# Kernel tuning notes

Measured on AMD Instinct MI355X. Metric: run time of the kernel, lower is better.

## Reference

```python
import math
import jax, jax.numpy as jnp
import numpy as np
from jax import lax

# (new_dilation, init_dilation) per layer for layers=3, blocks=2, kernel_size=2
DILATIONS = [(1, 1), (2, 1), (4, 2), (1, 4), (2, 1), (4, 2)]
K = 2  # kernel_size


def dilate(x, dilation, init_dilation):
    """Faithful port of the pad+permute+view+permute trick. x: (n, c, l)."""
    n, c, l = x.shape
    f = dilation / init_dilation
    if f == 1:
        return x
    new_l = int(math.ceil(l / f) * f)
    if new_l != l:
        x = jnp.pad(x, ((0, 0), (0, 0), (new_l - l, 0)))  # pad_start=True
        l = new_l
    l_new = int(math.ceil(l * init_dilation / dilation))
    n_new = int(math.ceil(n * dilation / init_dilation))
    x = jnp.transpose(x, (1, 2, 0)).reshape(c, l_new, n_new)
    return jnp.transpose(x, (2, 0, 1))


def conv2(x, w):
    """1D conv, kernel_size=2, no bias. x:(n,i,l), w:(o,i,2) -> (n,o,l-1)."""
    return (jnp.einsum('oi,nil->nol', w[:, :, 0], x[:, :, :-1])
            + jnp.einsum('oi,nil->nol', w[:, :, 1], x[:, :, 1:]))


def conv1x1(x, w):
    return jnp.einsum('oi,nil->nol', w, x)


def maxpool3s2(x):
    return lax.reduce_window(x, -jnp.inf, lax.max, (1, 1, 3), (1, 1, 2), 'VALID')


def wavenet_logits(x, start_w, filter_w, gate_w, res_w, skip_w,
                   end1_w, end1_b, end2_w, end2_b,
                   fc_w1, fc_b1, fc_w2, fc_b2, fc_w3, fc_b3):
    h = conv1x1(x, start_w)
    skip = None
    for i, (d, idil) in enumerate(DILATIONS):
        residual = dilate(h, d, idil)
        filt = jnp.tanh(conv2(residual, filter_w[i]))
        gate = jax.nn.sigmoid(conv2(residual, gate_w[i]))
        h = filt * gate
        s = h if h.shape[2] == 1 else dilate(h, 1, d)
        s = conv1x1(s, skip_w[i])
        if skip is None:
            skip = s
        else:
            skip = s + skip[:, :, -s.shape[2]:]
        h = conv1x1(h, res_w[i]) + residual[:, :, K - 1:]
    y = jax.nn.relu(skip)                                   # (B, 256, 1272)
    y = jax.nn.relu(conv1x1(y, end1_w) + end1_b[None, :, None])
    y = maxpool3s2(y)                                       # (B, 128, 635)
    y = jax.nn.relu(conv1x1(y, end2_w) + end2_b[None, :, None])
    y = maxpool3s2(y)                                       # (B, 32, 317)
    y = y.reshape(y.shape[0], -1)                           # (B, 10144)
    # output_layer MLP (dropout = identity in eval)
    y = jax.nn.relu(y @ fc_w1.T + fc_b1)
    y = jax.nn.relu(y @ fc_w2.T + fc_b2)
    return y @ fc_w3.T + fc_b3                              # (B, num_classes)


def setup_inputs() -> dict:
    key = jax.random.key(0)
    ks = jax.random.split(key, 12)
    f32 = jnp.float32

    def w(k, shape, fan_in):
        return jax.random.normal(k, shape, f32) / np.sqrt(fan_in).astype(np.float32)

    B, Cin, L = 256, 5, 1280
    return {
        'x': jax.random.normal(ks[0], (B, Cin, L), f32),
        'start_w': w(ks[1], (32, 5), 5),
        'filter_w': w(ks[2], (6, 32, 32, 2), 64),
        'gate_w': w(ks[3], (6, 32, 32, 2), 64),
        'res_w': w(ks[4], (6, 32, 32), 32),
        'skip_w': w(ks[5], (6, 256, 32), 32),
        'end1_w': w(ks[6], (128, 256), 256), 'end1_b': jnp.zeros((128,), f32),
        'end2_w': w(ks[7], (32, 128), 128), 'end2_b': jnp.zeros((32,), f32),
        'fc_w1': w(ks[8], (1024, 10144), 10144), 'fc_b1': jnp.zeros((1024,), f32),
        'fc_w2': w(ks[9], (256, 1024), 1024), 'fc_b2': jnp.zeros((256,), f32),
        'fc_w3': w(ks[10], (2, 256), 256), 'fc_b3': jnp.zeros((2,), f32),
    }


def reference(x, start_w, filter_w, gate_w, res_w, skip_w,
              end1_w, end1_b, end2_w, end2_b,
              fc_w1, fc_b1, fc_w2, fc_b2, fc_w3, fc_b3):
    logits = wavenet_logits(x, start_w, filter_w, gate_w, res_w, skip_w,
                            end1_w, end1_b, end2_w, end2_b,
                            fc_w1, fc_b1, fc_w2, fc_b2, fc_w3, fc_b3)
    y_prob = jax.nn.softmax(logits, axis=1)
    y_hat = jnp.argmax(logits, axis=1)
    return logits, y_prob, y_hat
```

## Files before the change

### kernel.cpp

```cpp
#include <hip/hip_runtime.h>
#include <math.h>


#define MCAP 327680

typedef short v8s __attribute__((ext_vector_type(8)));
typedef float v4f __attribute__((ext_vector_type(4)));

static inline long lmax_(long a, long b) { return a > b ? a : b; }

__device__ inline unsigned short rnbf(float x) {
    unsigned u = __float_as_uint(x);
    return (unsigned short)((u + 0x7FFFu + ((u >> 16) & 1u)) >> 16);
}
__device__ inline void split2(float v, unsigned short& h, unsigned short& l) {
    h = rnbf(v);
    const float hf = __uint_as_float(((unsigned)h) << 16);
    l = rnbf(v - hf);
}
__device__ inline unsigned packsplit(float v) {
    unsigned short h, l;
    split2(v, h, l);
    return ((unsigned)l << 16) | (unsigned)h;
}
__device__ inline float unpack2f(unsigned v) {
    return __uint_as_float(v << 16) + __uint_as_float(v & 0xffff0000u);
}

__global__ __launch_bounds__(256) void k_zero(float* __restrict__ p, int n) {
    int i = blockIdx.x * 256 + threadIdx.x;
    if (i < n) p[i] = 0.f;
}

__global__ __launch_bounds__(256) void k_start(const float* __restrict__ x,
                                               const float* __restrict__ sw,
                                               unsigned* __restrict__ h0) {
    int j = blockIdx.x * 256 + threadIdx.x;
    int t = j >> 8, n = j & 255;
    float xv[5];
#pragma unroll
    for (int i = 0; i < 5; ++i) xv[i] = x[n * 6400 + i * 1280 + t];
#pragma unroll
    for (int o = 0; o < 32; ++o) {
        float acc = 0.f;
#pragma unroll
        for (int i = 0; i < 5; ++i) acc = fmaf(sw[o * 5 + i], xv[i], acc);
        h0[o * MCAP + j] = packsplit(acc);
    }
}

__global__ __launch_bounds__(256) void k_prep(const float* __restrict__ skw,
                                              const float* __restrict__ e1w,
                                              const float* __restrict__ fw,
                                              const float* __restrict__ gw,
                                              const float* __restrict__ rw,
                                              const float* __restrict__ e2w,
                                              unsigned short* __restrict__ swt_hi,
                                              unsigned short* __restrict__ swt_lo,
                                              unsigned short* __restrict__ e1t_hi,
                                              unsigned short* __restrict__ e1t_lo,
                                              unsigned short* __restrict__ wfg_hi,
                                              unsigned short* __restrict__ wfg_lo,
                                              unsigned short* __restrict__ wr_hi,
                                              unsigned short* __restrict__ wr_lo,
                                              unsigned short* __restrict__ e2s_hi,
                                              unsigned short* __restrict__ e2s_lo) {
    int idx = blockIdx.x * 256 + threadIdx.x;
    if (idx < 49152) {
        int ch = idx / 192, k = idx - ch * 192;
        int l = k >> 5, i = k & 31;
        unsigned short h, lo;
        split2(skw[l * 8192 + ch * 32 + i], h, lo);
        swt_hi[idx] = h; swt_lo[idx] = lo;
    }
    if (idx < 32768) {
        int co = idx >> 8, kn = idx & 255;
        int hf = kn >> 7, wv = (kn >> 5) & 3, c = (kn >> 4) & 1, r = kn & 15;
        int ch = wv * 64 + (hf * 2 + c) * 16 + r;
        unsigned short h, lo;
        split2(e1w[co * 256 + ch], h, lo);
        e1t_hi[idx] = h; e1t_lo[idx] = lo;
    }
    if (idx < 24576) {
        int l = idx >> 12, r = idx & 4095;
        int row = r >> 6, k = r & 63;
        int o = row & 31, i = k & 31, tap = k >> 5;
        const float* src = (row < 32) ? fw : gw;
        unsigned short h, lo;
        split2(src[l * 2048 + o * 64 + i * 2 + tap], h, lo);
        wfg_hi[idx] = h; wfg_lo[idx] = lo;
    }
    if (idx < 12288) {
        int l = idx >> 11, r = idx & 2047;
        int o = r >> 6, k = r & 63, i = k & 31;
        unsigned short h, lo;
        split2(rw[l * 1024 + o * 32 + i], h, lo);
        wr_hi[idx] = h; wr_lo[idx] = lo;
    }
    if (idx < 4096) {
        unsigned short h, lo;
        split2(e2w[idx], h, lo);
        e2s_hi[idx] = h; e2s_lo[idx] = lo;
    }
}

__global__ __launch_bounds__(256) void k_prep_w1(const float* __restrict__ w1,
                                                 unsigned short* __restrict__ hi,
                                                 unsigned short* __restrict__ lo) {
    int idx = blockIdx.x * 256 + threadIdx.x;
    if (idx < 10387456) {
        unsigned short h, l;
        split2(w1[idx], h, l);
        hi[idx] = h; lo[idx] = l;
    }
}

__global__ __launch_bounds__(256) void k_layer_m(
    const unsigned* __restrict__ hin, const int hinBase, const int hinStride,
    unsigned* __restrict__ hout, const int houtBase, const int houtStride,
    unsigned* __restrict__ gsl, const int gStride,
    const unsigned short* __restrict__ wfg_hi, const unsigned short* __restrict__ wfg_lo,
    const unsigned short* __restrict__ wr_hi, const unsigned short* __restrict__ wr_lo,
    const int Jlo, const int NpmP, const int padN,
    const int so_, const int M0, const int M1, const int doRes)
{
    __shared__ unsigned short U[128 * 136];
    unsigned short* AT = U;
    unsigned short* GT = U;

    const int tid = threadIdx.x;
    const int j0 = Jlo + blockIdx.x * 128;

    {
        const int col = tid & 127;
        const int kg = tid >> 7;
        unsigned short* bh = &AT[col * 136 + kg * 32];
        unsigned short* bl = &AT[col * 136 + 64 + kg * 32];
        if (kg == 0 && j0 < padN) {
            uint4 z; z.x = z.y = z.z = z.w = 0u;
#pragma unroll
            for (int ch = 0; ch < 32; ch += 8) {
                *(uint4*)&bh[ch] = z;
                *(uint4*)&bl[ch] = z;
            }
        } else {
            const int off = (kg == 0) ? (j0 - padN) : (j0 + NpmP);
            const unsigned* p = hin + (off - hinBase) + col;
#pragma unroll
            for (int ch = 0; ch < 32; ch += 8) {
                alignas(16) unsigned short h8[8], l8[8];
#pragma unroll
                for (int u = 0; u < 8; ++u) {
                    const unsigned v = p[(size_t)(ch + u) * hinStride];
                    h8[u] = (unsigned short)(v & 0xffffu);
                    l8[u] = (unsigned short)(v >> 16);
                }
                *(uint4*)&bh[ch] = *(uint4*)h8;
                *(uint4*)&bl[ch] = *(uint4*)l8;
            }
        }
    }
    __syncthreads();

    const int lane = tid & 63;
    const int w    = tid >> 6;
    const int ch2  = w >> 1;
    const int mh   = w & 1;
    const int l15  = lane & 15;
    const int quad = lane >> 4;
    const int q8   = quad * 8;
    const int colb = ch2 * 64;

    v4f accf[4], accg[4];
#pragma unroll
    for (int nt = 0; nt < 4; ++nt) { accf[nt] = (v4f)(0.f); accg[nt] = (v4f)(0.f); }

#pragma unroll
    for (int kt = 0; kt < 2; ++kt) {
        const int frow = (mh * 16 + l15) * 64 + kt * 32 + q8;
        const int grow = (32 + mh * 16 + l15) * 64 + kt * 32 + q8;
        const v8s afh = *(const v8s*)&wfg_hi[frow];
        const v8s afl = *(const v8s*)&wfg_lo[frow];
        const v8s agh = *(const v8s*)&wfg_hi[grow];
        const v8s agl = *(const v8s*)&wfg_lo[grow];
#pragma unroll
        for (int nt = 0; nt < 4; ++nt) {
            const int col = colb + nt * 16 + l15;
            const v8s bh = *(const v8s*)&AT[col * 136 + kt * 32 + q8];
            const v8s bl = *(const v8s*)&AT[col * 136 + 64 + kt * 32 + q8];
            accf[nt] = __builtin_amdgcn_mfma_f32_16x16x32_bf16(afh, bh, accf[nt], 0, 0, 0);
            accf[nt] = __builtin_amdgcn_mfma_f32_16x16x32_bf16(afh, bl, accf[nt], 0, 0, 0);
            accf[nt] = __builtin_amdgcn_mfma_f32_16x16x32_bf16(afl, bh, accf[nt], 0, 0, 0);
            accg[nt] = __builtin_amdgcn_mfma_f32_16x16x32_bf16(agh, bh, accg[nt], 0, 0, 0);
            accg[nt] = __builtin_amdgcn_mfma_f32_16x16x32_bf16(agh, bl, accg[nt], 0, 0, 0);
            accg[nt] = __builtin_amdgcn_mfma_f32_16x16x32_bf16(agl, bh, accg[nt], 0, 0, 0);
        }
    }

    unsigned short gh[4][4], gl[4][4];
#pragma unroll
    for (int nt = 0; nt < 4; ++nt)
#pragma unroll
        for (int r = 0; r < 4; ++r) {
            const float f = accf[nt][r];
            const float g = accg[nt][r];
            const float th = 1.f - 2.f / (__expf(2.f * f) + 1.f);
            const float sg = 1.f / (1.f + __expf(-g));
            split2(th * sg, gh[nt][r], gl[nt][r]);
        }

    const int m0c = j0 - so_;
    if (m0c >= M0 && m0c < M1) {
#pragma unroll
        for (int nt = 0; nt < 4; ++nt)
#pragma unroll
            for (int r = 0; r < 4; ++r) {
                const int ch = mh * 16 + quad * 4 + r;
                const int m = (m0c - M0) + colb + nt * 16 + l15;
                gsl[(size_t)ch * gStride + m] =
                    ((unsigned)gl[nt][r] << 16) | (unsigned)gh[nt][r];
            }
    }

    if (doRes) {
        __syncthreads();
#pragma unroll
        for (int nt = 0; nt < 4; ++nt)
#pragma unroll
            for (int r = 0; r < 4; ++r) {
                const int ch = mh * 16 + quad * 4 + r;
                const int col = colb + nt * 16 + l15;
                GT[col * 72 + ch] = gh[nt][r];
                GT[col * 72 + 32 + ch] = gl[nt][r];
            }
        __syncthreads();

        v4f accr[4];
#pragma unroll
        for (int nt = 0; nt < 4; ++nt) accr[nt] = (v4f)(0.f);
#pragma unroll
        for (int kt = 0; kt < 2; ++kt) {
            const int row = (mh * 16 + l15) * 64 + kt * 32 + q8;
            const v8s arh = *(const v8s*)&wr_hi[row];
            const v8s arl = *(const v8s*)&wr_lo[row];
#pragma unroll
            for (int nt = 0; nt < 4; ++nt) {
                const int col = colb + nt * 16 + l15;
                const v8s b = *(const v8s*)&GT[col * 72 + kt * 32 + q8];
                accr[nt] = __builtin_amdgcn_mfma_f32_16x16x32_bf16(arh, b, accr[nt], 0, 0, 0);
                accr[nt] = __builtin_amdgcn_mfma_f32_16x16x32_bf16(arl, b, accr[nt], 0, 0, 0);
            }
        }

        const unsigned* tp = hin + (j0 + NpmP - hinBase);
#pragma unroll
        for (int nt = 0; nt < 4; ++nt)
#pragma unroll
            for (int r = 0; r < 4; ++r) {
                const int o = mh * 16 + quad * 4 + r;
                const int col = colb + nt * 16 + l15;
                const float tap1 = unpack2f(tp[(size_t)o * hinStride + col]);
                hout[(size_t)o * houtStride + (j0 - houtBase) + col] =
                    packsplit(accr[nt][r] + tap1);
            }
    }
}

__global__ __launch_bounds__(256, 4) void k_skip_end1_m(
    const unsigned* __restrict__ g,
    const unsigned short* __restrict__ swt_hi, const unsigned short* __restrict__ swt_lo,
    const unsigned short* __restrict__ e1t_hi, const unsigned short* __restrict__ e1t_lo,
    const float* __restrict__ b1, float* __restrict__ y1, const int gs)
{
    __shared__ unsigned short U[17408];
    unsigned short* gt_hi = U;
    unsigned short* gt_lo = U + 6656;
    unsigned short* st_hi = U;
    unsigned short* st_lo = U + 8704;

    const int tid  = threadIdx.x;
    const int m0   = blockIdx.x * 64;
    const int lane = tid & 63;
    const int w    = tid >> 6;
    const int l15  = lane & 15;
    const int q8   = (lane >> 4) * 8;
    const int rbase = (lane >> 4) * 4;

    const int scol = tid & 63;
    const int ks0  = (tid >> 6) * 8;

    v4f acc1[4][4];
#pragma unroll
    for (int a = 0; a < 4; ++a)
#pragma unroll
        for (int b = 0; b < 4; ++b) acc1[a][b] = (v4f)(0.f);

#pragma unroll
    for (int ph = 0; ph < 2; ++ph) {
        for (int kc = 0; kc < 96; kc += 32) {
            alignas(16) unsigned short h8[8], l8[8];
#pragma unroll
            for (int j = 0; j < 8; ++j) {
                const int k = ph * 96 + kc + ks0 + j;
                const unsigned v = g[(size_t)(k >> 5) * 32 * gs + (size_t)(k & 31) * gs + m0 + scol];
                h8[j] = (unsigned short)(v & 0xffffu);
                l8[j] = (unsigned short)(v >> 16);
            }
            *(v8s*)&gt_hi[scol * 104 + kc + ks0] = *(v8s*)h8;
            *(v8s*)&gt_lo[scol * 104 + kc + ks0] = *(v8s*)l8;
        }
        __syncthreads();

        for (int kc = 0; kc < 96; kc += 32) {
            v8s ah[4], al[4], bh[4], bl[4];
#pragma unroll
            for (int t = 0; t < 4; ++t) {
                const int row = (w * 64 + t * 16 + l15) * 192 + ph * 96 + kc + q8;
                ah[t] = *(const v8s*)&swt_hi[row];
                al[t] = *(const v8s*)&swt_lo[row];
                const int bo = (t * 16 + l15) * 104 + kc + q8;
                bh[t] = *(const v8s*)&gt_hi[bo];
                bl[t] = *(const v8s*)&gt_lo[bo];
            }
#pragma unroll
            for (int ct = 0; ct < 4; ++ct)
#pragma unroll
                for (int nt = 0; nt < 4; ++nt) {
                    acc1[ct][nt] = __builtin_amdgcn_mfma_f32_16x16x32_bf16(ah[ct], bh[nt], acc1[ct][nt], 0, 0, 0);
                    acc1[ct][nt] = __builtin_amdgcn_mfma_f32_16x16x32_bf16(ah[ct], bl[nt], acc1[ct][nt], 0, 0, 0);
                    acc1[ct][nt] = __builtin_amdgcn_mfma_f32_16x16x32_bf16(al[ct], bh[nt], acc1[ct][nt], 0, 0, 0);
                }
        }
        __syncthreads();
    }

    v4f acc2[2][4];
#pragma unroll
    for (int a = 0; a < 2; ++a)
#pragma unroll
        for (int b = 0; b < 4; ++b) acc2[a][b] = (v4f)(0.f);

#pragma unroll
    for (int hh = 0; hh < 2; ++hh) {
#pragma unroll
        for (int c2 = 0; c2 < 2; ++c2) {
            const int ct = hh * 2 + c2;
#pragma unroll
            for (int nt = 0; nt < 4; ++nt) {
                alignas(8) unsigned short sh[4], sl[4];
#pragma unroll
                for (int r = 0; r < 4; ++r) {
                    const float v = fmaxf(acc1[ct][nt][r], 0.f);
                    split2(v, sh[r], sl[r]);
                }
                const int ci  = w * 32 + c2 * 16 + rbase;
                const int col = nt * 16 + l15;
                *(uint2*)&st_hi[col * 136 + ci] = *(uint2*)sh;
                *(uint2*)&st_lo[col * 136 + ci] = *(uint2*)sl;
            }
        }
        __syncthreads();

        for (int kc = 0; kc < 128; kc += 32) {
            v8s ah2[2], al2[2], bh2[4], bl2[4];
#pragma unroll
            for (int t = 0; t < 2; ++t) {
                const int row = (w * 32 + t * 16 + l15) * 256 + hh * 128 + kc + q8;
                ah2[t] = *(const v8s*)&e1t_hi[row];
                al2[t] = *(const v8s*)&e1t_lo[row];
            }
#pragma unroll
            for (int t = 0; t < 4; ++t) {
                const int bo = (t * 16 + l15) * 136 + kc + q8;
                bh2[t] = *(const v8s*)&st_hi[bo];
                bl2[t] = *(const v8s*)&st_lo[bo];
            }
#pragma unroll
            for (int ct = 0; ct < 2; ++ct)
#pragma unroll
                for (int nt = 0; nt < 4; ++nt) {
                    acc2[ct][nt] = __builtin_amdgcn_mfma_f32_16x16x32_bf16(ah2[ct], bh2[nt], acc2[ct][nt], 0, 0, 0);
                    acc2[ct][nt] = __builtin_amdgcn_mfma_f32_16x16x32_bf16(ah2[ct], bl2[nt], acc2[ct][nt], 0, 0, 0);
                    acc2[ct][nt] = __builtin_amdgcn_mfma_f32_16x16x32_bf16(al2[ct], bh2[nt], acc2[ct][nt], 0, 0, 0);
                }
        }
        if (hh == 0) __syncthreads();
    }

#pragma unroll
    for (int ct = 0; ct < 2; ++ct) {
        const int cobase = w * 32 + ct * 16 + rbase;
        float bb[4];
#pragma unroll
        for (int r = 0; r < 4; ++r) bb[r] = b1[cobase + r];
#pragma unroll
        for (int nt = 0; nt < 4; ++nt) {
            const int col = m0 + nt * 16 + l15;
#pragma unroll
            for (int r = 0; r < 4; ++r)
                y1[(size_t)(cobase + r) * gs + col] = fmaxf(acc2[ct][nt][r] + bb[r], 0.f);
        }
    }
}

__global__ __launch_bounds__(256) void k_pe2_m(
    const float* __restrict__ y1c,
    const unsigned short* __restrict__ e2s_hi, const unsigned short* __restrict__ e2s_lo,
    const float* __restrict__ b2, float* __restrict__ e2c,
    const int gs, const int p1s)
{
    __shared__ unsigned short SP[2 * 64 * 136];
    unsigned short* sp_hi = SP;
    unsigned short* sp_lo = SP + 64 * 136;

    const int tid = threadIdx.x;
    const int m0 = blockIdx.x * 64;
    const int tp = m0 >> 8;
    const int nb = m0 & 255;

    {
        const int col = tid & 63;
        const int cig = tid >> 6;
        const int base = 2 * tp * 256 + nb + col;
#pragma unroll
        for (int u8 = 0; u8 < 4; ++u8) {
            alignas(16) unsigned short h8[8], l8[8];
#pragma unroll
            for (int u = 0; u < 8; ++u) {
                const int ci = cig * 32 + u8 * 8 + u;
                const float* yp = y1c + (size_t)ci * gs + base;
                const float v = fmaxf(fmaxf(yp[0], yp[256]), yp[512]);
                split2(v, h8[u], l8[u]);
            }
            *(uint4*)&sp_hi[col * 136 + cig * 32 + u8 * 8] = *(uint4*)h8;
            *(uint4*)&sp_lo[col * 136 + cig * 32 + u8 * 8] = *(uint4*)l8;
        }
    }
    __syncthreads();

    const int lane = tid & 63;
    const int w    = tid >> 6;
    const int mh   = w & 1;
    const int colh = w >> 1;
    const int l15  = lane & 15;
    const int quad = lane >> 4;
    const int q8   = quad * 8;

    v4f acc[2];
    acc[0] = (v4f)(0.f); acc[1] = (v4f)(0.f);

#pragma unroll
    for (int kc = 0; kc < 128; kc += 32) {
        const int row = (mh * 16 + l15) * 128 + kc + q8;
        const v8s ah = *(const v8s*)&e2s_hi[row];
        const v8s al = *(const v8s*)&e2s_lo[row];
#pragma unroll
        for (int nt = 0; nt < 2; ++nt) {
            const int col = colh * 32 + nt * 16 + l15;
            const v8s bh = *(const v8s*)&sp_hi[col * 136 + kc + q8];
            const v8s bl = *(const v8s*)&sp_lo[col * 136 + kc + q8];
            acc[nt] = __builtin_amdgcn_mfma_f32_16x16x32_bf16(ah, bh, acc[nt], 0, 0, 0);
            acc[nt] = __builtin_amdgcn_mfma_f32_16x16x32_bf16(ah, bl, acc[nt], 0, 0, 0);
            acc[nt] = __builtin_amdgcn_mfma_f32_16x16x32_bf16(al, bh, acc[nt], 0, 0, 0);
        }
    }

#pragma unroll
    for (int nt = 0; nt < 2; ++nt)
#pragma unroll
        for (int r = 0; r < 4; ++r) {
            const int co = mh * 16 + quad * 4 + r;
            const int col = m0 + colh * 32 + nt * 16 + l15;
            e2c[(size_t)co * p1s + col] = fmaxf(acc[nt][r] + b2[co], 0.f);
        }
}

__global__ __launch_bounds__(256) void k_pool2p(const float* __restrict__ e2c,
                                                unsigned* __restrict__ p2,
                                                const int p1s, const int A) {
    const int n = threadIdx.x, tl2 = blockIdx.x, co = blockIdx.y;
    const int base = co * p1s + tl2 * 512 + n;
    float v = fmaxf(fmaxf(e2c[base], e2c[base + 256]), e2c[base + 512]);
    p2[co * 81152 + (A + tl2) * 256 + n] = packsplit(v);
}

__global__ __launch_bounds__(256) void k_fc1_m(
    const unsigned short* __restrict__ w1s_hi, const unsigned short* __restrict__ w1s_lo,
    const unsigned* __restrict__ p2u, float* __restrict__ out)
{
    __shared__ unsigned short SB[2 * 64 * 40];
    unsigned short* sb_hi = SB;
    unsigned short* sb_lo = SB + 64 * 40;

    const int tid = threadIdx.x;
    const int o0 = blockIdx.x * 64;
    const int b0 = blockIdx.y * 64;
    const int k0 = blockIdx.z * 1280;
    const int kend = (k0 + 1280 < 10144) ? (k0 + 1280) : 10144;
    const int nch = (kend - k0) >> 5;

    const int lane = tid & 63;
    const int w    = tid >> 6;
    const int l15  = lane & 15;
    const int quad = lane >> 4;
    const int q8   = quad * 8;
    const int scol = tid & 63;
    const int kq   = tid >> 6;

    v4f acc[4];
#pragma unroll
    for (int nt = 0; nt < 4; ++nt) acc[nt] = (v4f)(0.f);

    for (int c = 0; c < nch; ++c) {
        const int kc = k0 + c * 32;
        alignas(16) unsigned short h8[8], l8[8];
#pragma unroll
        for (int j = 0; j < 8; ++j) {
            const unsigned v = p2u[(size_t)(kc + kq * 8 + j) * 256 + b0 + scol];
            h8[j] = (unsigned short)(v & 0xffffu);
            l8[j] = (unsigned short)(v >> 16);
        }
        __syncthreads();
        *(v8s*)&sb_hi[scol * 40 + kq * 8] = *(v8s*)h8;
        *(v8s*)&sb_lo[scol * 40 + kq * 8] = *(v8s*)l8;
        __syncthreads();

        const int arow = (o0 + w * 16 + l15) * 10144 + kc + q8;
        const v8s ah = *(const v8s*)&w1s_hi[arow];
        const v8s al = *(const v8s*)&w1s_lo[arow];
#pragma unroll
        for (int nt = 0; nt < 4; ++nt) {
            const v8s bh = *(const v8s*)&sb_hi[(nt * 16 + l15) * 40 + q8];
            const v8s bl = *(const v8s*)&sb_lo[(nt * 16 + l15) * 40 + q8];
            acc[nt] = __builtin_amdgcn_mfma_f32_16x16x32_bf16(ah, bh, acc[nt], 0, 0, 0);
            acc[nt] = __builtin_amdgcn_mfma_f32_16x16x32_bf16(ah, bl, acc[nt], 0, 0, 0);
            acc[nt] = __builtin_amdgcn_mfma_f32_16x16x32_bf16(al, bh, acc[nt], 0, 0, 0);
        }
    }

#pragma unroll
    for (int nt = 0; nt < 4; ++nt)
#pragma unroll
        for (int r = 0; r < 4; ++r)
            atomicAdd(&out[(size_t)(o0 + w * 16 + quad * 4 + r) * 256 + b0 + nt * 16 + l15],
                      acc[nt][r]);
}

__global__ __launch_bounds__(256) void k_gemm64(const float* __restrict__ A,
                                                const float* __restrict__ B,
                                                float* __restrict__ C,
                                                const int Ktot, const int KC) {
    __shared__ float sA[32 * 65];
    __shared__ float sB[32 * 68];

    const int tid = threadIdx.x;
    const int o0 = blockIdx.x * 64;
    const int b0 = blockIdx.y * 64;
    const int k0 = blockIdx.z * KC;

    float acc[4][4];
#pragma unroll
    for (int i = 0; i < 4; ++i)
#pragma unroll
        for (int jq = 0; jq < 4; ++jq) acc[i][jq] = 0.f;

    const int ao  = tid >> 2;
    const int ak8 = (tid & 3) * 8;
    const int bk  = tid >> 3;
    const int bb8 = (tid & 7) * 8;
    const int to4 = (tid & 15) * 4;
    const int tb4 = (tid >> 4) * 4;

    for (int kc = 0; kc < KC; kc += 32) {
        const int kcLen = (KC - kc < 32) ? (KC - kc) : 32;
        const float* ap = A + (size_t)(o0 + ao) * Ktot + k0 + kc + ak8;
#pragma unroll
        for (int i = 0; i < 8; ++i) {
            float v = (ak8 + i < kcLen) ? ap[i] : 0.f;
            sA[(ak8 + i) * 65 + ao] = v;
        }
        if (bk < kcLen) {
            const float* bp = B + (size_t)(k0 + kc + bk) * 256 + b0 + bb8;
            const float4 v0 = *(const float4*)bp;
            const float4 v1 = *(const float4*)(bp + 4);
            *(float4*)&sB[bk * 68 + bb8] = v0;
            *(float4*)&sB[bk * 68 + bb8 + 4] = v1;
        } else {
            float4 z; z.x = z.y = z.z = z.w = 0.f;
            *(float4*)&sB[bk * 68 + bb8] = z;
            *(float4*)&sB[bk * 68 + bb8 + 4] = z;
        }
        __syncthreads();

#pragma unroll 8
        for (int kk = 0; kk < 32; ++kk) {
            const float4 av = *(const float4*)&sA[kk * 65 + to4];
            const float4 bv = *(const float4*)&sB[kk * 68 + tb4];
            const float aa[4] = {av.x, av.y, av.z, av.w};
#pragma unroll
            for (int i = 0; i < 4; ++i) {
                acc[i][0] = fmaf(aa[i], bv.x, acc[i][0]);
                acc[i][1] = fmaf(aa[i], bv.y, acc[i][1]);
                acc[i][2] = fmaf(aa[i], bv.z, acc[i][2]);
                acc[i][3] = fmaf(aa[i], bv.w, acc[i][3]);
            }
        }
        __syncthreads();
    }

#pragma unroll
    for (int i = 0; i < 4; ++i)
#pragma unroll
        for (int jq = 0; jq < 4; ++jq)
            atomicAdd(&C[(size_t)(o0 + to4 + i) * 256 + b0 + tb4 + jq], acc[i][jq]);
}

__global__ __launch_bounds__(256) void k_actbias(const float* __restrict__ raw,
                                                 const float* __restrict__ bias,
                                                 float* __restrict__ out) {
    const int k = blockIdx.x, b = threadIdx.x;
    out[k * 256 + b] = fmaxf(raw[k * 256 + b] + bias[k], 0.f);
}

__global__ __launch_bounds__(256) void k_fc3(const float* __restrict__ fc2raw,
                                             const float* __restrict__ fb2,
                                             const float* __restrict__ w3,
                                             const float* __restrict__ b3,
                                             float* __restrict__ out) {
    const int b = threadIdx.x;
    float l0 = b3[0], l1 = b3[1];
    for (int k = 0; k < 256; ++k) {
        const float a = fmaxf(fc2raw[k * 256 + b] + fb2[k], 0.f);
        l0 = fmaf(w3[k], a, l0);
        l1 = fmaf(w3[256 + k], a, l1);
    }
    out[2 * b] = l0;
    out[2 * b + 1] = l1;
    const float mx = fmaxf(l0, l1);
    const float e0 = expf(l0 - mx), e1 = expf(l1 - mx);
    const float inv = 1.f / (e0 + e1);
    out[512 + 2 * b] = e0 * inv;
    out[513 + 2 * b] = e1 * inv;
    out[1024 + b] = (l1 > l0) ? 1.f : 0.f;
}

extern "C" void kernel_launch(void* const* d_in, const int* in_sizes, int n_in,
                              void* d_out, int out_size, void* d_ws, size_t ws_size,
                              hipStream_t stream) {
    const float* x        = (const float*)d_in[0];
    const float* start_w  = (const float*)d_in[1];
    const float* filter_w = (const float*)d_in[2];
    const float* gate_w   = (const float*)d_in[3];
    const float* res_w    = (const float*)d_in[4];
    const float* skip_w   = (const float*)d_in[5];
    const float* e1w      = (const float*)d_in[6];
    const float* e1b      = (const float*)d_in[7];
    const float* e2w      = (const float*)d_in[8];
    const float* e2b      = (const float*)d_in[9];
    const float* w1       = (const float*)d_in[10];
    const float* fb1      = (const float*)d_in[11];
    const float* w2       = (const float*)d_in[12];
    const float* fb2      = (const float*)d_in[13];
    const float* w3       = (const float*)d_in[14];
    const float* b3       = (const float*)d_in[15];

    float* ws = (float*)d_ws;

    const long o_h0   = 0;
    const long o_p2   = 10485760;
    const long o_fc1  = 13082624;
    const long o_fc2  = 13344768;
    const long o_wbf  = 13410304;
    const long o_wfg  = 13492224;
    const long o_wr   = 13516800;
    const long o_e2s  = 13529088;
    const long o_act1 = 13533184;
    const long o_w1s  = 13795328;
    const long o_G    = 24182784;

    long budget = (long)((double)ws_size * 0.94 / 4.0);
    int dB = 1;
    for (int d = 317; d >= 1; --d) {
        long mch = 256L * (4L * d + 3), hs = mch + 4096;
        long tot = o_G + 192L * mch + lmax_(128L * mch, 64L * hs);
        if (tot <= budget) { dB = d; break; }
    }
    int K = (317 + dB - 1) / dB;
    dB = (317 + K - 1) / K;
    const long MchA  = 256L * (4L * dB + 3);
    const long HSPAN = MchA + 4096;
    const long o_X   = o_G + 192L * MchA;
    const long P1S   = 256L * (2L * dB + 1);

    unsigned* h0 = (unsigned*)(ws + o_h0);
    unsigned* p2 = (unsigned*)(ws + o_p2);
    float* fc1r = ws + o_fc1;
    float* fc2r = ws + o_fc2;
    unsigned short* swt_hi = (unsigned short*)(ws + o_wbf);
    unsigned short* swt_lo = swt_hi + 49152;
    unsigned short* e1t_hi = swt_lo + 49152;
    unsigned short* e1t_lo = e1t_hi + 32768;
    unsigned short* wfg_hi = (unsigned short*)(ws + o_wfg);
    unsigned short* wfg_lo = wfg_hi + 24576;
    unsigned short* wr_hi  = (unsigned short*)(ws + o_wr);
    unsigned short* wr_lo  = wr_hi + 12288;
    unsigned short* e2s_hi = (unsigned short*)(ws + o_e2s);
    unsigned short* e2s_lo = e2s_hi + 4096;
    unsigned short* w1s_hi = (unsigned short*)(ws + o_w1s);
    unsigned short* w1s_lo = w1s_hi + 10387456;
    float* act1 = ws + o_act1;
    unsigned* G  = (unsigned*)(ws + o_G);
    unsigned* hA = (unsigned*)(ws + o_X);
    unsigned* hB = (unsigned*)(ws + o_X) + 32L * HSPAN;
    float* y1c  = ws + o_X;
    float* e2c  = ws + o_G;

    k_zero<<<1280, 256, 0, stream>>>(fc1r, 327680);
    k_start<<<1280, 256, 0, stream>>>(x, start_w, h0);
    k_prep<<<192, 256, 0, stream>>>(skip_w, e1w, filter_w, gate_w, res_w, e2w,
                                    swt_hi, swt_lo, e1t_hi, e1t_lo,
                                    wfg_hi, wfg_lo, wr_hi, wr_lo,
                                    e2s_hi, e2s_lo);
    k_prep_w1<<<40576, 256, 0, stream>>>(w1, w1s_hi, w1s_lo);

    const int Mc[6]   = {327424, 327168, 326656, 326400, 326144, 325632};
    const int NpmP[6] = {256, 256, 512, 256, 256, 512};
    const int pN[6]   = {0, 256, 512, 0, 256, 512};
    const int so_[6]  = {1792, 1536, 1024, 768, 512, 0};
    const int JloO[6] = {-1536, -1280, -768, -768, -512, 0};

    for (int c = 0; c < K; ++c) {
        const int A = c * dB;
        int B = A + dB; if (B > 317) B = 317;
        const int dBc = B - A;
        const int M0 = 1024 * A;
        int tmax = 4 * B + 3; if (tmax > 1272) tmax = 1272;
        const int Tt = tmax - 4 * A;
        const int M1 = M0 + 256 * Tt;

        int Jlo[6], Jhi[6];
        for (int q = 0; q < 6; ++q) {
            int lo = M0 + JloO[q]; if (lo < 0) lo = 0;
            int hi = M1 + so_[q];  if (hi > Mc[q]) hi = Mc[q];
            Jlo[q] = lo; Jhi[q] = hi;
        }

        for (int q = 0; q < 6; ++q) {
            const unsigned* hin = (q == 0) ? h0 : ((q & 1) ? hA : hB);
            const int hinBase   = (q == 0) ? 0 : Jlo[q - 1];
            const int hinStride = (q == 0) ? MCAP : (int)HSPAN;
            unsigned* hout = (q & 1) ? hB : hA;
            const int Jcnt = Jhi[q] - Jlo[q];
            k_layer_m<<<Jcnt / 128, 256, 0, stream>>>(
                hin, hinBase, hinStride, hout, Jlo[q], (int)HSPAN,
                G + (long)q * 32 * MchA, (int)MchA,
                wfg_hi + q * 4096, wfg_lo + q * 4096,
                wr_hi + q * 2048, wr_lo + q * 2048,
                Jlo[q], NpmP[q], pN[q], so_[q], M0, M1, (q < 5) ? 1 : 0);
        }

        const int Mchc = 256 * Tt;
        k_skip_end1_m<<<Mchc / 64, 256, 0, stream>>>(
            G, swt_hi, swt_lo, e1t_hi, e1t_lo, e1b, y1c, (int)MchA);
        const int T1c = 2 * dBc + 1;
        k_pe2_m<<<T1c * 4, 256, 0, stream>>>(
            y1c, e2s_hi, e2s_lo, e2b, e2c, (int)MchA, (int)P1S);
        k_pool2p<<<dim3(dBc, 32), 256, 0, stream>>>(e2c, p2, (int)P1S, A);
    }

    k_fc1_m<<<dim3(16, 4, 8), 256, 0, stream>>>(w1s_hi, w1s_lo, p2, fc1r);
    k_actbias<<<1024, 256, 0, stream>>>(fc1r, fb1, act1);
    k_gemm64<<<dim3(4, 4, 4), 256, 0, stream>>>(w2, act1, fc2r, 1024, 256);
    k_fc3<<<1, 256, 0, stream>>>(fc2r, fb2, w3, b3, (float*)d_out);
}
```

Before: 868.8 us.

## Store gated activations in pre-tiled bf16 layout for direct LDS loading

The layer kernel now stages gated outputs through shared memory and writes them as contiguous 64-column tiles, with hi/lo bf16 planes interleaved in the layout the skip/end1 kernel wants. The skip/end1 kernel then pulls its whole tile into LDS with global_load_lds async copies, replacing the strided per-element gather and unpacking. This removes uncoalesced global reads and one sync pair per phase. In exchange it enlarges LDS use, lowers the occupancy hint from 4 to 3, adds barriers to every layer launch, and slightly enlarges the G workspace.

```diff
diff --git a/kernel.cpp b/kernel.cpp
--- a/kernel.cpp
+++ b/kernel.cpp
@@ -118,7 +118,7 @@
 __global__ __launch_bounds__(256) void k_layer_m(
     const unsigned* __restrict__ hin, const int hinBase, const int hinStride,
     unsigned* __restrict__ hout, const int houtBase, const int houtStride,
-    unsigned* __restrict__ gsl, const int gStride,
+    unsigned short* __restrict__ Gt, const int phs,
     const unsigned short* __restrict__ wfg_hi, const unsigned short* __restrict__ wfg_lo,
     const unsigned short* __restrict__ wr_hi, const unsigned short* __restrict__ wr_lo,
     const int Jlo, const int NpmP, const int padN,
@@ -209,32 +209,37 @@
             split2(th * sg, gh[nt][r], gl[nt][r]);
         }
 
+    __syncthreads();
+#pragma unroll
+    for (int nt = 0; nt < 4; ++nt)
+#pragma unroll
+        for (int r = 0; r < 4; ++r) {
+            const int ch = mh * 16 + quad * 4 + r;
+            const int col = colb + nt * 16 + l15;
+            GT[col * 72 + ch] = gh[nt][r];
+            GT[col * 72 + 32 + ch] = gl[nt][r];
+        }
+    __syncthreads();
+
     const int m0c = j0 - so_;
     if (m0c >= M0 && m0c < M1) {
-#pragma unroll
-        for (int nt = 0; nt < 4; ++nt)
-#pragma unroll
-            for (int r = 0; r < 4; ++r) {
-                const int ch = mh * 16 + quad * 4 + r;
-                const int m = (m0c - M0) + colb + nt * 16 + l15;
-                gsl[(size_t)ch * gStride + m] =
-                    ((unsigned)gl[nt][r] << 16) | (unsigned)gh[nt][r];
-            }
+        const int b0 = (m0c - M0) >> 6;
+        const int colc = tid >> 1;
+        const int hf = tid & 1;
+        const unsigned short* src = &GT[colc * 72 + hf * 32];
+        const v8s r0 = *(const v8s*)(src);
+        const v8s r1 = *(const v8s*)(src + 8);
+        const v8s r2 = *(const v8s*)(src + 16);
+        const v8s r3 = *(const v8s*)(src + 24);
+        unsigned short* dst = Gt + (size_t)(b0 + (colc >> 6)) * 25600 + phs
+                              + (size_t)(colc & 63) * 200 + hf * 32;
+        *(v8s*)(dst) = r0;
+        *(v8s*)(dst + 8) = r1;
+        *(v8s*)(dst + 16) = r2;
+        *(v8s*)(dst + 24) = r3;
     }
 
     if (doRes) {
-        __syncthreads();
-#pragma unroll
-        for (int nt = 0; nt < 4; ++nt)
-#pragma unroll
-            for (int r = 0; r < 4; ++r) {
-                const int ch = mh * 16 + quad * 4 + r;
-                const int col = colb + nt * 16 + l15;
-                GT[col * 72 + ch] = gh[nt][r];
-                GT[col * 72 + 32 + ch] = gl[nt][r];
-            }
-        __syncthreads();
-
         v4f accr[4];
 #pragma unroll
         for (int nt = 0; nt < 4; ++nt) accr[nt] = (v4f)(0.f);
@@ -266,15 +271,13 @@
     }
 }
 
-__global__ __launch_bounds__(256, 4) void k_skip_end1_m(
-    const unsigned* __restrict__ g,
+__global__ __launch_bounds__(256, 3) void k_skip_end1_m(
+    const unsigned short* __restrict__ Gt,
     const unsigned short* __restrict__ swt_hi, const unsigned short* __restrict__ swt_lo,
     const unsigned short* __restrict__ e1t_hi, const unsigned short* __restrict__ e1t_lo,
     const float* __restrict__ b1, float* __restrict__ y1, const int gs)
 {
-    __shared__ unsigned short U[17408];
-    unsigned short* gt_hi = U;
-    unsigned short* gt_lo = U + 6656;
+    __shared__ unsigned short U[25600];
     unsigned short* st_hi = U;
     unsigned short* st_lo = U + 8704;
 
@@ -286,8 +289,19 @@
     const int q8   = (lane >> 4) * 8;
     const int rbase = (lane >> 4) * 4;
 
-    const int scol = tid & 63;
-    const int ks0  = (tid >> 6) * 8;
+    {
+        const unsigned short* gsrc = Gt + (size_t)blockIdx.x * 25600;
+#pragma unroll
+        for (int r = 0; r < 12; ++r)
+            __builtin_amdgcn_global_load_lds(
+                (const unsigned*)(gsrc + r * 2048 + tid * 8),
+                (unsigned*)(&U[r * 2048 + tid * 8]), 16, 0, 0);
+        if (tid < 128)
+            __builtin_amdgcn_global_load_lds(
+                (const unsigned*)(gsrc + 24576 + tid * 8),
+                (unsigned*)(&U[24576 + tid * 8]), 16, 0, 0);
+    }
+    __syncthreads();
 
     v4f acc1[4][4];
 #pragma unroll
@@ -297,42 +311,40 @@
 
 #pragma unroll
     for (int ph = 0; ph < 2; ++ph) {
+        const unsigned short* gtp = U + ph * 12800;
         for (int kc = 0; kc < 96; kc += 32) {
-            alignas(16) unsigned short h8[8], l8[8];
-#pragma unroll
-            for (int j = 0; j < 8; ++j) {
-                const int k = ph * 96 + kc + ks0 + j;
-                const unsigned v = g[(size_t)(k >> 5) * 32 * gs + (size_t)(k & 31) * gs + m0 + scol];
-                h8[j] = (unsigned short)(v & 0xffffu);
-                l8[j] = (unsigned short)(v >> 16);
-            }
-            *(v8s*)&gt_hi[scol * 104 + kc + ks0] = *(v8s*)h8;
-            *(v8s*)&gt_lo[scol * 104 + kc + ks0] = *(v8s*)l8;
-        }
-        __syncthreads();
-
-        for (int kc = 0; kc < 96; kc += 32) {
-            v8s ah[4], al[4], bh[4], bl[4];
+            const int so = (kc >> 5) * 64;
+            v8s bh[4], bl[4];
 #pragma unroll
             for (int t = 0; t < 4; ++t) {
-                const int row = (w * 64 + t * 16 + l15) * 192 + ph * 96 + kc + q8;
-                ah[t] = *(const v8s*)&swt_hi[row];
-                al[t] = *(const v8s*)&swt_lo[row];
-                const int bo = (t * 16 + l15) * 104 + kc + q8;
-                bh[t] = *(const v8s*)&gt_hi[bo];
-                bl[t] = *(const v8s*)&gt_lo[bo];
-            }
-#pragma unroll
-            for (int ct = 0; ct < 4; ++ct)
-#pragma unroll
-                for (int nt = 0; nt < 4; ++nt) {
-                    acc1[ct][nt] = __builtin_amdgcn_mfma_f32_16x16x32_bf16(ah[ct], bh[nt], acc1[ct][nt], 0, 0, 0);
-                    acc1[ct][nt] = __builtin_amdgcn_mfma_f32_16x16x32_bf16(ah[ct], bl[nt], acc1[ct][nt], 0, 0, 0);
-                    acc1[ct][nt] = __builtin_amdgcn_mfma_f32_16x16x32_bf16(al[ct], bh[nt], acc1[ct][nt], 0, 0, 0);
+                const unsigned short* bp = &gtp[(t * 16 + l15) * 200 + so + q8];
+                bh[t] = *(const v8s*)bp;
+                bl[t] = *(const v8s*)(bp + 32);
+            }
+#pragma unroll
+            for (int cp = 0; cp < 2; ++cp) {
+                v8s ah[2], al[2];
+#pragma unroll
+                for (int u = 0; u < 2; ++u) {
+                    const int ct = cp * 2 + u;
+                    const int row = (w * 64 + ct * 16 + l15) * 192 + ph * 96 + kc + q8;
+                    ah[u] = *(const v8s*)&swt_hi[row];
+                    al[u] = *(const v8s*)&swt_lo[row];
                 }
-        }
-        __syncthreads();
-    }
+#pragma unroll
+                for (int u = 0; u < 2; ++u) {
+                    const int ct = cp * 2 + u;
+#pragma unroll
+                    for (int nt = 0; nt < 4; ++nt) {
+                        acc1[ct][nt] = __builtin_amdgcn_mfma_f32_16x16x32_bf16(ah[u], bh[nt], acc1[ct][nt], 0, 0, 0);
+                        acc1[ct][nt] = __builtin_amdgcn_mfma_f32_16x16x32_bf16(ah[u], bl[nt], acc1[ct][nt], 0, 0, 0);
+                        acc1[ct][nt] = __builtin_amdgcn_mfma_f32_16x16x32_bf16(al[u], bh[nt], acc1[ct][nt], 0, 0, 0);
+                    }
+                }
+            }
+        }
+    }
+    __syncthreads();
 
     v4f acc2[2][4];
 #pragma unroll
@@ -682,14 +694,14 @@
     int dB = 1;
     for (int d = 317; d >= 1; --d) {
         long mch = 256L * (4L * d + 3), hs = mch + 4096;
-        long tot = o_G + 192L * mch + lmax_(128L * mch, 64L * hs);
+        long tot = o_G + 200L * mch + lmax_(128L * mch, 64L * hs);
         if (tot <= budget) { dB = d; break; }
     }
     int K = (317 + dB - 1) / dB;
     dB = (317 + K - 1) / K;
     const long MchA  = 256L * (4L * dB + 3);
     const long HSPAN = MchA + 4096;
-    const long o_X   = o_G + 192L * MchA;
+    const long o_X   = o_G + 200L * MchA;
     const long P1S   = 256L * (2L * dB + 1);
 
     unsigned* h0 = (unsigned*)(ws + o_h0);
@@ -709,7 +721,7 @@
     unsigned short* w1s_hi = (unsigned short*)(ws + o_w1s);
     unsigned short* w1s_lo = w1s_hi + 10387456;
     float* act1 = ws + o_act1;
-    unsigned* G  = (unsigned*)(ws + o_G);
+    unsigned short* Gt = (unsigned short*)(ws + o_G);
     unsigned* hA = (unsigned*)(ws + o_X);
     unsigned* hB = (unsigned*)(ws + o_X) + 32L * HSPAN;
     float* y1c  = ws + o_X;
@@ -751,9 +763,10 @@
             const int hinStride = (q == 0) ? MCAP : (int)HSPAN;
             unsigned* hout = (q & 1) ? hB : hA;
             const int Jcnt = Jhi[q] - Jlo[q];
+            const int phs = (q / 3) * 12800 + (q % 3) * 64;
             k_layer_m<<<Jcnt / 128, 256, 0, stream>>>(
                 hin, hinBase, hinStride, hout, Jlo[q], (int)HSPAN,
-                G + (long)q * 32 * MchA, (int)MchA,
+                Gt, phs,
                 wfg_hi + q * 4096, wfg_lo + q * 4096,
                 wr_hi + q * 2048, wr_lo + q * 2048,
                 Jlo[q], NpmP[q], pN[q], so_[q], M0, M1, (q < 5) ? 1 : 0);
@@ -761,7 +774,7 @@
 
         const int Mchc = 256 * Tt;
         k_skip_end1_m<<<Mchc / 64, 256, 0, stream>>>(
-            G, swt_hi, swt_lo, e1t_hi, e1t_lo, e1b, y1c, (int)MchA);
+            Gt, swt_hi, swt_lo, e1t_hi, e1t_lo, e1b, y1c, (int)MchA);
         const int T1c = 2 * dBc + 1;
         k_pe2_m<<<T1c * 4, 256, 0, stream>>>(
             y1c, e2s_hi, e2s_lo, e2b, e2c, (int)MchA, (int)P1S);
```

Result: slower. 906.6 us (+4.3%).
